# Performance work log

Hardware: AMD Instinct MI355X
Metric: run time of the kernel (lower is better)

Reference implementation:

```python
import jax, jax.numpy as jnp
from jax import lax
import numpy as np

T = 8192
D = 10000
L_CONV = T - 18          # after two valid convs with kernel 10
L_POOL = L_CONV // 2     # after MaxPool1d(2)
FLAT = 128 * L_POOL      # flattened feature size fed to the on-the-fly Linear
TWO_PI = 6.283185307179586

# feat indices used by feat_emb[0..17], in emb order
FEAT_IDX = np.array([558, 582, 554, 552, 93, 555, 580, 571, 574, 578,
                     566, 287, 556, 550, 14, 551, 64, 581], dtype=np.int32)


def setup_inputs() -> dict:
    key = jax.random.key(0)
    ks = jax.random.split(key, 12)
    inp = {
        "signals": jax.random.normal(ks[0], (T, 4), jnp.float32),
        "feat": jax.random.normal(ks[1], (600,), jnp.float32),
        "conv1_w": jax.random.normal(ks[2], (64, 4, 10), jnp.float32) * 0.15,
        "conv1_b": jax.random.normal(ks[3], (64,), jnp.float32) * 0.05,
        "conv2_w": jax.random.normal(ks[4], (128, 64, 10), jnp.float32) * 0.04,
        "conv2_b": jax.random.normal(ks[5], (128,), jnp.float32) * 0.05,
        "lin_w": jax.random.normal(ks[6], (128, FLAT), jnp.float32) * (1.0 / np.sqrt(FLAT)),
        "lin_b": jax.random.normal(ks[7], (128,), jnp.float32) * 0.05,
        "hdc_w": jax.random.normal(ks[8], (D, 128), jnp.float32),  # Sinusoid weight ~ N(0,1)
        "hdc_b": jax.random.uniform(ks[9], (D,), jnp.float32, 0.0, TWO_PI),
        "feat_w": jax.random.normal(ks[10], (18, D), jnp.float32),  # 18 Sinusoid(1, D) weights
        "feat_b": jax.random.uniform(ks[11], (18, D), jnp.float32, 0.0, TWO_PI),
        "feat_idx": jnp.asarray(FEAT_IDX),
    }
    return inp


def _sinusoid(proj, bias):
    # torchhd Sinusoid: cos(xW^T + b) * sin(xW^T)
    return jnp.cos(proj + bias) * jnp.sin(proj)


def reference(signals, feat, conv1_w, conv1_b, conv2_w, conv2_b,
              lin_w, lin_b, hdc_w, hdc_b, feat_w, feat_b, feat_idx):
    # CNN front-end (dropout is identity in eval mode)
    x = signals.T[None]  # [1, 4, T]
    dn = ('NCH', 'OIH', 'NCH')
    x = lax.conv_general_dilated(x, conv1_w, (1,), 'VALID', dimension_numbers=dn)
    x = jax.nn.relu(x + conv1_b[None, :, None])
    x = lax.conv_general_dilated(x, conv2_w, (1,), 'VALID', dimension_numbers=dn)
    x = jax.nn.relu(x + conv2_b[None, :, None])  # [1, 128, L_CONV]
    L = x.shape[2] // 2
    x = x[:, :, :L * 2].reshape(1, 128, L, 2).max(axis=-1)  # MaxPool1d(2)
    x = x.reshape(1, -1)                                     # [1, FLAT]
    x = jax.nn.relu(x @ lin_w.T + lin_b)                     # [1, 128]

    # sample hypervector
    proj = x @ hdc_w.T                                       # [1, D]
    sample_hv = _sinusoid(proj, hdc_b)

    # 18 per-feature sinusoid embeddings, vectorized: proj_i = feat[idx_i] * w_i
    fvals = feat[feat_idx]                                   # [18]
    fproj = fvals[:, None] * feat_w                          # [18, D]
    h = _sinusoid(fproj, feat_b)                             # [18, D]

    feat_hv = ((h[14] + h[11]) * h[16]
               * (h[4] + h[8] + h[6] + h[1] + h[5] + h[12] + h[17])
               * h[13] * (h[15] + h[2]) * h[3]
               * h[0] * h[10] * h[7] * h[9])                 # [D]

    combined = sample_hv + feat_hv[None]                     # [1, D]
    quantized = jnp.where(combined > 0, 1.0, -1.0).astype(combined.dtype)
    return quantized.reshape(-1)                             # [D]
```

## Files before the change

### kernel.cpp

```cpp
#include <hip/hip_runtime.h>
#include <math.h>

#define T_IN    8192
#define T1      8183
#define T2      8174
#define LP      4087
#define NFLAT   523136
#define NFLAT4  130784
#define NDIM    10000
#define RSTRIDE 8208
#define F_OFF   (64*RSTRIDE)
#define P_OFF   (F_OFF + NFLAT)
#define NCHUNK  32
#define CHUNK4  4087

typedef __attribute__((ext_vector_type(4))) float f4;

__global__ __launch_bounds__(256) void k1_conv1(
    const float* __restrict__ sig, const float* __restrict__ w1,
    const float* __restrict__ b1, float* __restrict__ r1)
{
  __shared__ float4 srow[266];
  const int tid = threadIdx.x;
  const int t0b = blockIdx.x * 256;
  for (int idx = tid; idx < 266; idx += 256) {
    int t = t0b + idx;
    float4 v = make_float4(0.f, 0.f, 0.f, 0.f);
    if (t < T_IN) v = ((const float4*)sig)[t];
    srow[idx] = v;
  }
  __syncthreads();
  const int t = t0b + tid;
  float s[40];
#pragma unroll
  for (int k = 0; k < 10; ++k) {
    float4 v = srow[tid + k];
    s[4*k+0] = v.x; s[4*k+1] = v.y; s[4*k+2] = v.z; s[4*k+3] = v.w;
  }
  const int c0 = blockIdx.y * 8;
  for (int c = c0; c < c0 + 8; ++c) {
    const float* __restrict__ w = w1 + c * 40;
    float a0 = 0.f, a1 = 0.f, a2 = 0.f, a3 = 0.f;
#pragma unroll
    for (int k = 0; k < 10; ++k) {
      a0 = fmaf(s[4*k+0], w[k     ], a0);
      a1 = fmaf(s[4*k+1], w[10 + k], a1);
      a2 = fmaf(s[4*k+2], w[20 + k], a2);
      a3 = fmaf(s[4*k+3], w[30 + k], a3);
    }
    float v = fmaxf((a0 + a1) + (a2 + a3) + b1[c], 0.f);
    if (t < T1) r1[c * RSTRIDE + t] = v;
  }
}

__global__ __launch_bounds__(256) void k2_conv2pool(
    const float* __restrict__ r1, const float* __restrict__ w2,
    const float* __restrict__ b2, float* __restrict__ flat)
{
  __shared__ float tile[16][272];
  const int tid  = threadIdx.x;
  const int lane = tid & 63;
  const int wave = tid >> 6;
  const int t0b  = blockIdx.x * 256;
  const int o0   = __builtin_amdgcn_readfirstlane(blockIdx.y * 8 + wave * 2);
  const int t0   = t0b + lane * 4;

  float acc[2][4];
#pragma unroll
  for (int a = 0; a < 2; ++a)
#pragma unroll
    for (int b = 0; b < 4; ++b) acc[a][b] = 0.f;

  for (int cc = 0; cc < 4; ++cc) {
    __syncthreads();
#pragma unroll
    for (int rr = 0; rr < 4; ++rr) {
      int row = wave * 4 + rr;
      const float4* src = (const float4*)(r1 + (cc * 16 + row) * RSTRIDE + t0b);
      ((float4*)&tile[row][0])[lane] = src[lane];
      if (lane < 4) ((float4*)&tile[row][0])[64 + lane] = src[64 + lane];
    }
    __syncthreads();

    for (int cr = 0; cr < 16; ++cr) {
      float f[16];
      const float4* tr4 = (const float4*)&tile[cr][0];
#pragma unroll
      for (int q = 0; q < 4; ++q) {
        float4 v = tr4[lane + q];
        f[4*q+0] = v.x; f[4*q+1] = v.y; f[4*q+2] = v.z; f[4*q+3] = v.w;
      }
      const int c = cc * 16 + cr;
#pragma unroll
      for (int oo = 0; oo < 2; ++oo) {
        const float* __restrict__ w = w2 + ((o0 + oo) * 64 + c) * 10;
#pragma unroll
        for (int k = 0; k < 10; ++k) {
          float wv = w[k];
#pragma unroll
          for (int tt = 0; tt < 4; ++tt)
            acc[oo][tt] = fmaf(wv, f[k + tt], acc[oo][tt]);
        }
      }
    }
  }

#pragma unroll
  for (int oo = 0; oo < 2; ++oo) {
    const int o = o0 + oo;
    const float bias = b2[o];
#pragma unroll
    for (int lt = 0; lt < 2; ++lt) {
      float a = acc[oo][2*lt]     + bias;
      float b = acc[oo][2*lt + 1] + bias;
      float m = fmaxf(fmaxf(a, b), 0.f);
      int l = t0 / 2 + lt;
      if (l < LP) flat[o * LP + l] = m;
    }
  }
}

__global__ __launch_bounds__(256) void k3_linear(
    const float* __restrict__ lw, const float* __restrict__ flat,
    float* __restrict__ partials)
{
  const int tid = threadIdx.x;
  const int ch  = blockIdx.x;
  const int j0  = blockIdx.y * 4;
  const f4* __restrict__ fl = (const f4*)flat + (size_t)ch * CHUNK4;

  float r[4];
#pragma unroll
  for (int ph = 0; ph < 2; ++ph) {
    const int j = j0 + 2 * ph;
    const f4* __restrict__ p0 = (const f4*)lw + (size_t)(j + 0) * NFLAT4 + (size_t)ch * CHUNK4;
    const f4* __restrict__ p1 = (const f4*)lw + (size_t)(j + 1) * NFLAT4 + (size_t)ch * CHUNK4;
    f4 a0 = (f4)0.f, a1 = (f4)0.f;
    for (int i = tid; i < CHUNK4; i += 256) {
      f4 x  = fl[i];
      f4 w0 = p0[i];
      f4 w1 = p1[i];
      a0.x = fmaf(x.x, w0.x, a0.x); a0.y = fmaf(x.y, w0.y, a0.y);
      a0.z = fmaf(x.z, w0.z, a0.z); a0.w = fmaf(x.w, w0.w, a0.w);
      a1.x = fmaf(x.x, w1.x, a1.x); a1.y = fmaf(x.y, w1.y, a1.y);
      a1.z = fmaf(x.z, w1.z, a1.z); a1.w = fmaf(x.w, w1.w, a1.w);
    }
    r[2*ph + 0] = (a0.x + a0.y) + (a0.z + a0.w);
    r[2*ph + 1] = (a1.x + a1.y) + (a1.z + a1.w);
  }

  __shared__ float red[4][257];
#pragma unroll
  for (int j = 0; j < 4; ++j) red[j][tid] = r[j];
  for (int off = 128; off > 0; off >>= 1) {
    __syncthreads();
    if (tid < off) {
#pragma unroll
      for (int j = 0; j < 4; ++j) red[j][tid] += red[j][tid + off];
    }
  }
  if (tid == 0) {
#pragma unroll
    for (int j = 0; j < 4; ++j) partials[(j0 + j) * NCHUNK + ch] = red[j][0];
  }
}

__global__ __launch_bounds__(64) void k4_hdc(
    const float* __restrict__ partials, const float* __restrict__ lin_b,
    const float* __restrict__ hdc_w, const float* __restrict__ hdc_b,
    const float* __restrict__ feat, const int* __restrict__ feat_idx,
    const float* __restrict__ feat_w, const float* __restrict__ feat_b,
    float* __restrict__ out)
{
  __shared__ __align__(16) float y[128];
  __shared__ float fv[18];
  const int tid = threadIdx.x;
#pragma unroll
  for (int half = 0; half < 2; ++half) {
    const int row = tid + half * 64;
    float s = lin_b[row];
    const float* p = partials + row * NCHUNK;
#pragma unroll
    for (int c = 0; c < NCHUNK; ++c) s += p[c];
    y[row] = fmaxf(s, 0.f);
  }
  if (tid < 18) fv[tid] = feat[feat_idx[tid]];
  __syncthreads();

  const int d = blockIdx.x * 64 + tid;
  if (d >= NDIM) return;

  const float4* __restrict__ hw = (const float4*)(hdc_w + d * 128);
  const float4* __restrict__ yy = (const float4*)y;
  float4 ac = make_float4(0, 0, 0, 0);
#pragma unroll
  for (int q = 0; q < 32; ++q) {
    float4 w = hw[q];
    float4 v = yy[q];
    ac.x = fmaf(w.x, v.x, ac.x); ac.y = fmaf(w.y, v.y, ac.y);
    ac.z = fmaf(w.z, v.z, ac.z); ac.w = fmaf(w.w, v.w, ac.w);
  }
  const float proj = (ac.x + ac.y) + (ac.z + ac.w);
  const float sample_hv = cosf(proj + hdc_b[d]) * sinf(proj);

  float h[18];
#pragma unroll
  for (int i = 0; i < 18; ++i) {
    float fp = fv[i] * feat_w[i * NDIM + d];
    h[i] = cosf(fp + feat_b[i * NDIM + d]) * sinf(fp);
  }
  const float feat_hv =
      (h[14] + h[11]) * h[16]
    * (h[4] + h[8] + h[6] + h[1] + h[5] + h[12] + h[17])
    * h[13] * (h[15] + h[2]) * h[3]
    * h[0] * h[10] * h[7] * h[9];

  const float comb = sample_hv + feat_hv;
  out[d] = comb > 0.f ? 1.f : -1.f;
}

extern "C" void kernel_launch(void* const* d_in, const int* in_sizes, int n_in,
                              void* d_out, int out_size, void* d_ws, size_t ws_size,
                              hipStream_t stream)
{
  const float* sig  = (const float*)d_in[0];
  const float* feat = (const float*)d_in[1];
  const float* w1   = (const float*)d_in[2];
  const float* b1   = (const float*)d_in[3];
  const float* w2   = (const float*)d_in[4];
  const float* b2   = (const float*)d_in[5];
  const float* lw   = (const float*)d_in[6];
  const float* lb   = (const float*)d_in[7];
  const float* hw   = (const float*)d_in[8];
  const float* hb   = (const float*)d_in[9];
  const float* fw   = (const float*)d_in[10];
  const float* fb   = (const float*)d_in[11];
  const int*   fidx = (const int*)d_in[12];
  float* out = (float*)d_out;
  float* ws  = (float*)d_ws;

  float* r1       = ws;
  float* flat     = ws + F_OFF;
  float* partials = ws + P_OFF;

  k1_conv1    <<<dim3(32, 8),  256, 0, stream>>>(sig, w1, b1, r1);
  k2_conv2pool<<<dim3(32, 16), 256, 0, stream>>>(r1, w2, b2, flat);
  k3_linear   <<<dim3(32, 32), 256, 0, stream>>>(lw, flat, partials);
  k4_hdc      <<<dim3(157, 1), 64,  0, stream>>>(partials, lb, hw, hb,
                                                 feat, fidx, fw, fb, out);
}
```

Baseline: 101.2 us.

## Stage conv2 weights in LDS, unroll linear loop, split HDC dot across lanes

The conv2 kernel now copies its block's 8 output channels of weights into shared memory, so inner-loop weight reads hit LDS instead of global/scalar loads. The linear kernel preloads the activation chunk into registers once, fully unrolls the 16-iteration loop with a guarded tail, and adds an occupancy hint to launch_bounds. The HDC kernel splits each 128-wide dot product across 4 lanes with shuffle reductions and launches 625 blocks instead of 157. That last change also makes all 4 lanes compute the 18 sinusoid features redundantly. In exchange the code uses more registers (64 floats for xr) and more LDS.

```diff
diff --git a/kernel.cpp b/kernel.cpp
--- a/kernel.cpp
+++ b/kernel.cpp
@@ -58,12 +58,20 @@
     const float* __restrict__ b2, float* __restrict__ flat)
 {
   __shared__ float tile[16][272];
+  __shared__ float wl[5120];
   const int tid  = threadIdx.x;
   const int lane = tid & 63;
   const int wave = tid >> 6;
   const int t0b  = blockIdx.x * 256;
-  const int o0   = __builtin_amdgcn_readfirstlane(blockIdx.y * 8 + wave * 2);
+  const int oBase = blockIdx.y * 8;
+  const int lc0  = __builtin_amdgcn_readfirstlane(wave * 2);
   const int t0   = t0b + lane * 4;
+
+  {
+    const float4* src = (const float4*)(w2 + oBase * 640);
+    float4* dst = (float4*)wl;
+    for (int i = tid; i < 1280; i += 256) dst[i] = src[i];
+  }
 
   float acc[2][4];
 #pragma unroll
@@ -93,7 +101,7 @@
       const int c = cc * 16 + cr;
 #pragma unroll
       for (int oo = 0; oo < 2; ++oo) {
-        const float* __restrict__ w = w2 + ((o0 + oo) * 64 + c) * 10;
+        const float* __restrict__ w = wl + ((lc0 + oo) * 64 + c) * 10;
 #pragma unroll
         for (int k = 0; k < 10; ++k) {
           float wv = w[k];
@@ -107,7 +115,7 @@
 
 #pragma unroll
   for (int oo = 0; oo < 2; ++oo) {
-    const int o = o0 + oo;
+    const int o = oBase + lc0 + oo;
     const float bias = b2[o];
 #pragma unroll
     for (int lt = 0; lt < 2; ++lt) {
@@ -120,7 +128,7 @@
   }
 }
 
-__global__ __launch_bounds__(256) void k3_linear(
+__global__ __launch_bounds__(256, 4) void k3_linear(
     const float* __restrict__ lw, const float* __restrict__ flat,
     float* __restrict__ partials)
 {
@@ -129,17 +137,27 @@
   const int j0  = blockIdx.y * 4;
   const f4* __restrict__ fl = (const f4*)flat + (size_t)ch * CHUNK4;
 
+  const bool lastOK = (tid + 15 * 256) < CHUNK4;
+  const int  iLast  = lastOK ? tid + 15 * 256 : 0;
+
+  f4 xr[16];
+#pragma unroll
+  for (int it = 0; it < 15; ++it) xr[it] = fl[tid + it * 256];
+  xr[15] = lastOK ? fl[iLast] : (f4)0.f;
+
   float r[4];
 #pragma unroll
   for (int ph = 0; ph < 2; ++ph) {
-    const int j = j0 + 2 * ph;
-    const f4* __restrict__ p0 = (const f4*)lw + (size_t)(j + 0) * NFLAT4 + (size_t)ch * CHUNK4;
-    const f4* __restrict__ p1 = (const f4*)lw + (size_t)(j + 1) * NFLAT4 + (size_t)ch * CHUNK4;
+    const f4* __restrict__ p0 = (const f4*)lw
+        + (size_t)(j0 + 2 * ph) * NFLAT4 + (size_t)ch * CHUNK4;
+    const f4* __restrict__ p1 = p0 + NFLAT4;
     f4 a0 = (f4)0.f, a1 = (f4)0.f;
-    for (int i = tid; i < CHUNK4; i += 256) {
-      f4 x  = fl[i];
+#pragma unroll
+    for (int it = 0; it < 16; ++it) {
+      const int i = (it < 15) ? (tid + it * 256) : iLast;
       f4 w0 = p0[i];
       f4 w1 = p1[i];
+      f4 x  = xr[it];
       a0.x = fmaf(x.x, w0.x, a0.x); a0.y = fmaf(x.y, w0.y, a0.y);
       a0.z = fmaf(x.z, w0.z, a0.z); a0.w = fmaf(x.w, w0.w, a0.w);
       a1.x = fmaf(x.x, w1.x, a1.x); a1.y = fmaf(x.y, w1.y, a1.y);
@@ -187,20 +205,25 @@
   if (tid < 18) fv[tid] = feat[feat_idx[tid]];
   __syncthreads();
 
-  const int d = blockIdx.x * 64 + tid;
-  if (d >= NDIM) return;
+  const int g = tid >> 2;
+  const int q = tid & 3;
+  const int d = blockIdx.x * 16 + g;
 
   const float4* __restrict__ hw = (const float4*)(hdc_w + d * 128);
   const float4* __restrict__ yy = (const float4*)y;
   float4 ac = make_float4(0, 0, 0, 0);
 #pragma unroll
-  for (int q = 0; q < 32; ++q) {
-    float4 w = hw[q];
-    float4 v = yy[q];
+  for (int it = 0; it < 8; ++it) {
+    const int idx = it * 4 + q;
+    float4 w = hw[idx];
+    float4 v = yy[idx];
     ac.x = fmaf(w.x, v.x, ac.x); ac.y = fmaf(w.y, v.y, ac.y);
     ac.z = fmaf(w.z, v.z, ac.z); ac.w = fmaf(w.w, v.w, ac.w);
   }
-  const float proj = (ac.x + ac.y) + (ac.z + ac.w);
+  float proj = (ac.x + ac.y) + (ac.z + ac.w);
+  proj += __shfl_xor(proj, 1);
+  proj += __shfl_xor(proj, 2);
+
   const float sample_hv = cosf(proj + hdc_b[d]) * sinf(proj);
 
   float h[18];
@@ -216,7 +239,7 @@
     * h[0] * h[10] * h[7] * h[9];
 
   const float comb = sample_hv + feat_hv;
-  out[d] = comb > 0.f ? 1.f : -1.f;
+  if (q == 0) out[d] = comb > 0.f ? 1.f : -1.f;
 }
 
 extern "C" void kernel_launch(void* const* d_in, const int* in_sizes, int n_in,
@@ -246,6 +269,6 @@
   k1_conv1    <<<dim3(32, 8),  256, 0, stream>>>(sig, w1, b1, r1);
   k2_conv2pool<<<dim3(32, 16), 256, 0, stream>>>(r1, w2, b2, flat);
   k3_linear   <<<dim3(32, 32), 256, 0, stream>>>(lw, flat, partials);
-  k4_hdc      <<<dim3(157, 1), 64,  0, stream>>>(partials, lb, hw, hb,
+  k4_hdc      <<<dim3(625, 1), 64,  0, stream>>>(partials, lb, hw, hb,
                                                  feat, fidx, fw, fb, out);
 }
```

After: 111.9 us. 10.6% more time.
